# Optimization experiments

Measured on AMD Instinct MI355X. Metric: run time of the kernel, lower is better.

The kernel has to match this reference:

```python
import jax, jax.numpy as jnp
import numpy as np

LEAKY_SLOPE = 0.2
DENSITY = 0.05


def setup_inputs() -> dict:
    key = jax.random.key(0)
    k1, k2, k3, k4, k5, k6 = jax.random.split(key, 6)
    N, F_in, F_out = 8192, 128, 64
    h = jax.random.normal(k1, (N, F_in), dtype=jnp.float32)
    # Linear(in, out, bias=False) weight is [out, in]
    W = jax.random.normal(k2, (F_out, F_in), dtype=jnp.float32) * (1.0 / np.sqrt(F_in))
    a_left = jax.random.normal(k3, (F_out,), dtype=jnp.float32) * 0.1
    a_right = jax.random.normal(k4, (F_out,), dtype=jnp.float32) * 0.1
    vals = jax.random.uniform(k5, (N, N), dtype=jnp.float32)
    keep = jax.random.uniform(k6, (N, N)) < DENSITY
    adj = jnp.where(keep, vals, 0.0)  # raw adjacency; self-loops added in reference
    return {"h": h, "W": W, "a_left": a_left, "a_right": a_right, "adj": adj}


def reference(h, W, a_left, a_right, adj):
    N = adj.shape[0]
    A = adj + jnp.eye(N, dtype=adj.dtype)          # A = adjacency + I (self-loops)
    mask = jnp.abs(A) > 0                          # valued-mask support
    Wh = h @ W.T                                   # [N, F_out]
    e_left = Wh @ a_left                           # [N]
    e_right = Wh @ a_right                         # [N]
    e = e_left[:, None] + e_right[None, :]         # [N, N] additive scores
    e = jnp.where(e >= 0, e, LEAKY_SLOPE * e)      # LeakyReLU(0.2)
    e = jnp.where(mask, e, -jnp.inf)               # masked_fill(mask==0, -inf)
    attention = jax.nn.softmax(e, axis=1) * A      # valued masking post-softmax
    # dropout p=0.0 -> identity (eval-mode reference)
    return attention @ Wh                          # [N, F_out]
```

## Files before the change

kernel.cpp:

```cpp
#include <hip/hip_runtime.h>
#include <hip/hip_bf16.h>
#include <hip/hip_fp16.h>

#define N    8192
#define FIN  128
#define FOUT 64
#define LEAKY 0.2f
#define CAPQ 256
#define LOG2E 1.44269504088896340736f

struct alignas(8) Ent { unsigned joff; float w; };

__global__ __launch_bounds__(256) void wh_eLR_kernel(
    const float* __restrict__ h, const float* __restrict__ Wm,
    const float* __restrict__ aL, const float* __restrict__ aR,
    __half* __restrict__ Whh, float* __restrict__ eL2, float* __restrict__ eR2)
{
    __shared__ float sW[FOUT][FIN + 1];
    __shared__ float sh[4][FIN];
    const int t = threadIdx.x;
    const int rbase = blockIdx.x * 4;

    for (int idx = t; idx < FOUT * FIN; idx += 256)
        sW[idx >> 7][idx & 127] = Wm[idx];
    for (int idx = t; idx < 4 * FIN; idx += 256)
        sh[idx >> 7][idx & 127] = h[(size_t)(rbase + (idx >> 7)) * FIN + (idx & 127)];
    __syncthreads();

    const int wv = t >> 6, f = t & 63;
    const int row = rbase + wv;
    float acc = 0.f;
    #pragma unroll 16
    for (int k = 0; k < FIN; ++k) acc += sh[wv][k] * sW[f][k];
    Whh[(size_t)row * FOUT + f] = __float2half_rn(acc);

    float vl = acc * aL[f];
    float vr = acc * aR[f];
    #pragma unroll
    for (int d = 32; d > 0; d >>= 1) {
        vl += __shfl_down(vl, d, 64);
        vr += __shfl_down(vr, d, 64);
    }
    if (f == 0) { eL2[row] = vl * LOG2E; eR2[row] = vr * LOG2E; }
}

__global__ __launch_bounds__(256, 8) void gat_row_kernel(
    const float* __restrict__ adj, const __half* __restrict__ Whh,
    const float* __restrict__ eL2p, const float* __restrict__ eR2p,
    float* __restrict__ out)
{
    __shared__ Ent ent[4][CAPQ];
    __shared__ float4 facc[4][16];
    __shared__ float fpsum[4];

    const int t = threadIdx.x;
    const int wv = t >> 6;
    const int lane = t & 63;
    const int row = blockIdx.x;

    const float el = eL2p[row];
    const float4* __restrict__ arow4 = (const float4*)(adj + (size_t)row * N);
    const char* __restrict__ er2b = (const char*)eR2p;
    const char* __restrict__ whb  = (const char*)Whh;
    Ent* __restrict__ myent = ent[wv];

    const unsigned l7 = ((unsigned)((wv << 11) + lane * 4)) << 7;
    const unsigned l7u[4] = {l7, l7 + 128, l7 + 256, l7 + 384};
    const unsigned row7 = ((unsigned)row) << 7;
    const int rcl = (row >> 8) - (wv << 3);
    const int qb = (wv << 9) + lane;

    int base = 0;

    #pragma unroll
    for (int half = 0; half < 2; ++half) {
        float4 b[4];
        #pragma unroll
        for (int c = 0; c < 4; ++c)
            b[c] = arow4[qb + (half * 4 + c) * 64];
        #pragma unroll
        for (int c = 0; c < 4; ++c) {
            const int cg = half * 4 + c;
            const float av[4] = {b[c].x, b[c].y, b[c].z, b[c].w};
            const unsigned cbits = ((unsigned)cg) << 15;
            const bool cdiag = (cg == rcl);
            #pragma unroll
            for (int u = 0; u < 4; ++u) {
                float a = av[u];
                if (cdiag) {
                    if ((cbits + l7u[u]) == row7) a += 1.0f;
                }
                const bool nz = (a != 0.f);
                const unsigned long long m = __ballot(nz);
                const int before = __builtin_amdgcn_mbcnt_hi(
                    (unsigned)(m >> 32),
                    __builtin_amdgcn_mbcnt_lo((unsigned)m, 0));
                if (nz) {
                    Ent e; e.joff = cbits + l7u[u]; e.w = a;
                    myent[base + before] = e;
                }
                base += (int)__popcll(m);
            }
        }
    }
    const int cnt = min(base, CAPQ - 16);
    if (lane < 16) { Ent z; z.joff = 0; z.w = 0.f; myent[cnt + lane] = z; }

    asm volatile("s_waitcnt lgkmcnt(0)" ::: "memory");

    const int g = lane >> 4;
    const int fb = (lane & 15) * 8;
    const int cnt16 = (cnt + 15) & ~15;
    float ax = 0.f, ay = 0.f, az = 0.f, aw = 0.f;
    float bx = 0.f, by = 0.f, bz = 0.f, bw = 0.f;
    float cx = 0.f, cy = 0.f, cz = 0.f, cw = 0.f;
    float dx = 0.f, dy = 0.f, dz = 0.f, dw = 0.f;
    float psum = 0.f;
    for (int k = g; k < cnt16; k += 16) {
        const Ent e0 = myent[k];
        const Ent e1 = myent[k + 4];
        const Ent e2 = myent[k + 8];
        const Ent e3 = myent[k + 12];
        const float er0 = *(const float*)(er2b + (e0.joff >> 5));
        const float er1 = *(const float*)(er2b + (e1.joff >> 5));
        const float er2 = *(const float*)(er2b + (e2.joff >> 5));
        const float er3 = *(const float*)(er2b + (e3.joff >> 5));
        const uint2 u0 = *(const uint2*)(whb + (e0.joff + fb));
        const uint2 u1 = *(const uint2*)(whb + (e1.joff + fb));
        const uint2 u2 = *(const uint2*)(whb + (e2.joff + fb));
        const uint2 u3 = *(const uint2*)(whb + (e3.joff + fb));
        float y0 = el + er0; y0 = fmaxf(y0, LEAKY * y0);
        float y1 = el + er1; y1 = fmaxf(y1, LEAKY * y1);
        float y2 = el + er2; y2 = fmaxf(y2, LEAKY * y2);
        float y3 = el + er3; y3 = fmaxf(y3, LEAKY * y3);
        const float p0 = exp2f(y0), p1 = exp2f(y1);
        const float p2 = exp2f(y2), p3 = exp2f(y3);
        psum += (e0.w != 0.f ? p0 : 0.f) + (e1.w != 0.f ? p1 : 0.f)
              + (e2.w != 0.f ? p2 : 0.f) + (e3.w != 0.f ? p3 : 0.f);
        const float w0 = p0 * e0.w, w1 = p1 * e1.w;
        const float w2 = p2 * e2.w, w3 = p3 * e3.w;
        const float2 f00 = __half22float2(*(const __half2*)&u0.x);
        const float2 f01 = __half22float2(*(const __half2*)&u0.y);
        const float2 f10 = __half22float2(*(const __half2*)&u1.x);
        const float2 f11 = __half22float2(*(const __half2*)&u1.y);
        const float2 f20 = __half22float2(*(const __half2*)&u2.x);
        const float2 f21 = __half22float2(*(const __half2*)&u2.y);
        const float2 f30 = __half22float2(*(const __half2*)&u3.x);
        const float2 f31 = __half22float2(*(const __half2*)&u3.y);
        ax += w0 * f00.x; ay += w0 * f00.y; az += w0 * f01.x; aw += w0 * f01.y;
        bx += w1 * f10.x; by += w1 * f10.y; bz += w1 * f11.x; bw += w1 * f11.y;
        cx += w2 * f20.x; cy += w2 * f20.y; cz += w2 * f21.x; cw += w2 * f21.y;
        dx += w3 * f30.x; dy += w3 * f30.y; dz += w3 * f31.x; dw += w3 * f31.y;
    }
    ax += bx; ay += by; az += bz; aw += bw;
    cx += dx; cy += dy; cz += dz; cw += dw;
    ax += cx; ay += cy; az += cz; aw += cw;
    #pragma unroll
    for (int d = 32; d >= 16; d >>= 1) {
        ax += __shfl_down(ax, d, 64);
        ay += __shfl_down(ay, d, 64);
        az += __shfl_down(az, d, 64);
        aw += __shfl_down(aw, d, 64);
        psum += __shfl_down(psum, d, 64);
    }
    if (lane < 16) { float4 p; p.x = ax; p.y = ay; p.z = az; p.w = aw; facc[wv][lane] = p; }
    if (lane == 0) fpsum[wv] = psum;
    __syncthreads();

    if (t < 16) {
        const float Z = fpsum[0] + fpsum[1] + fpsum[2] + fpsum[3];
        const float rz = 1.0f / Z;
        const float4 p0 = facc[0][t];
        const float4 p1 = facc[1][t];
        const float4 p2 = facc[2][t];
        const float4 p3 = facc[3][t];
        float4 r;
        r.x = (p0.x + p1.x + p2.x + p3.x) * rz;
        r.y = (p0.y + p1.y + p2.y + p3.y) * rz;
        r.z = (p0.z + p1.z + p2.z + p3.z) * rz;
        r.w = (p0.w + p1.w + p2.w + p3.w) * rz;
        *(float4*)(out + (size_t)row * FOUT + t * 4) = r;
    }
}

extern "C" void kernel_launch(void* const* d_in, const int* in_sizes, int n_in,
                              void* d_out, int out_size, void* d_ws, size_t ws_size,
                              hipStream_t stream) {
    const float* h   = (const float*)d_in[0];
    const float* Wm  = (const float*)d_in[1];
    const float* aL  = (const float*)d_in[2];
    const float* aR  = (const float*)d_in[3];
    const float* adj = (const float*)d_in[4];
    float* outp = (float*)d_out;

    __half* Whh = (__half*)d_ws;
    float* eL2  = (float*)((char*)d_ws + (size_t)N * FOUT * 2);
    float* eR2  = eL2 + N;

    wh_eLR_kernel<<<N / 4, 256, 0, stream>>>(h, Wm, aL, aR, Whh, eL2, eR2);
    gat_row_kernel<<<N, 256, 0, stream>>>(adj, Whh, eL2, eR2, outp);
}
```

Baseline: 77.02 us.

## Split adjacency compaction and attention gather into separate kernels via global lists

The fused per-row kernel is split in two. A compaction kernel streams the dense adjacency and writes per-wave nonzero lists and counts to workspace in global memory. A gather kernel then loads those lists into LDS and does the softmax-weighted aggregation. This separates the bandwidth-bound stream from the latency-bound gather so each kernel can run at its own occupancy. The cost is an extra launch and a global write and re-read of the lists (about 64 MB), and the code assumes the workspace is large enough to hold them.

```diff
diff --git a/kernel.cpp b/kernel.cpp
--- a/kernel.cpp
+++ b/kernel.cpp
@@ -44,25 +44,16 @@
     if (f == 0) { eL2[row] = vl * LOG2E; eR2[row] = vr * LOG2E; }
 }
 
-__global__ __launch_bounds__(256, 8) void gat_row_kernel(
-    const float* __restrict__ adj, const __half* __restrict__ Whh,
-    const float* __restrict__ eL2p, const float* __restrict__ eR2p,
-    float* __restrict__ out)
+__global__ __launch_bounds__(256, 8) void compact_kernel(
+    const float* __restrict__ adj, Ent* __restrict__ glist, int* __restrict__ gcnt)
 {
-    __shared__ Ent ent[4][CAPQ];
-    __shared__ float4 facc[4][16];
-    __shared__ float fpsum[4];
-
     const int t = threadIdx.x;
     const int wv = t >> 6;
     const int lane = t & 63;
     const int row = blockIdx.x;
 
-    const float el = eL2p[row];
     const float4* __restrict__ arow4 = (const float4*)(adj + (size_t)row * N);
-    const char* __restrict__ er2b = (const char*)eR2p;
-    const char* __restrict__ whb  = (const char*)Whh;
-    Ent* __restrict__ myent = ent[wv];
+    Ent* __restrict__ mylist = glist + ((size_t)row * 4 + wv) * CAPQ;
 
     const unsigned l7 = ((unsigned)((wv << 11) + lane * 4)) << 7;
     const unsigned l7u[4] = {l7, l7 + 128, l7 + 256, l7 + 384};
@@ -71,7 +62,6 @@
     const int qb = (wv << 9) + lane;
 
     int base = 0;
-
     #pragma unroll
     for (int half = 0; half < 2; ++half) {
         float4 b[4];
@@ -97,13 +87,37 @@
                     __builtin_amdgcn_mbcnt_lo((unsigned)m, 0));
                 if (nz) {
                     Ent e; e.joff = cbits + l7u[u]; e.w = a;
-                    myent[base + before] = e;
+                    mylist[base + before] = e;
                 }
                 base += (int)__popcll(m);
             }
         }
     }
-    const int cnt = min(base, CAPQ - 16);
+    if (lane == 0) gcnt[row * 4 + wv] = base;
+}
+
+__global__ __launch_bounds__(256, 8) void gather_kernel(
+    const Ent* __restrict__ glist, const int* __restrict__ gcnt,
+    const __half* __restrict__ Whh, const float* __restrict__ eL2p,
+    const float* __restrict__ eR2p, float* __restrict__ out)
+{
+    __shared__ Ent ent[4][CAPQ];
+    __shared__ float4 facc[4][16];
+    __shared__ float fpsum[4];
+
+    const int t = threadIdx.x;
+    const int wv = t >> 6;
+    const int lane = t & 63;
+    const int row = blockIdx.x;
+
+    const float el = eL2p[row];
+    const char* __restrict__ er2b = (const char*)eR2p;
+    const char* __restrict__ whb  = (const char*)Whh;
+    const Ent* __restrict__ mylist = glist + ((size_t)row * 4 + wv) * CAPQ;
+    Ent* __restrict__ myent = ent[wv];
+
+    const int cnt = min(gcnt[row * 4 + wv], CAPQ - 16);
+    for (int k = lane; k < cnt; k += 64) myent[k] = mylist[k];
     if (lane < 16) { Ent z; z.joff = 0; z.w = 0.f; myent[cnt + lane] = z; }
 
     asm volatile("s_waitcnt lgkmcnt(0)" ::: "memory");
@@ -193,10 +207,14 @@
     const float* adj = (const float*)d_in[4];
     float* outp = (float*)d_out;
 
-    __half* Whh = (__half*)d_ws;
-    float* eL2  = (float*)((char*)d_ws + (size_t)N * FOUT * 2);
+    char* ws = (char*)d_ws;
+    __half* Whh = (__half*)ws;
+    float* eL2  = (float*)(ws + (size_t)N * FOUT * 2);
     float* eR2  = eL2 + N;
+    int*   gcnt = (int*)(eR2 + N);
+    Ent*   glist = (Ent*)(gcnt + N * 4);
 
     wh_eLR_kernel<<<N / 4, 256, 0, stream>>>(h, Wm, aL, aR, Whh, eL2, eR2);
-    gat_row_kernel<<<N, 256, 0, stream>>>(adj, Whh, eL2, eR2, outp);
-}
+    compact_kernel<<<N, 256, 0, stream>>>(adj, glist, gcnt);
+    gather_kernel<<<N, 256, 0, stream>>>(glist, gcnt, Whh, eL2, eR2, outp);
+}
```

Measured after the change: 108.0 us. +40.2%, slower.
